# Performance work log

Measured on AMD Instinct MI355X. Metric: run time of the kernel, lower is better.

The kernel has to match this reference:

```python
import jax, jax.numpy as jnp
import numpy as np

B, N, D = 64, 256, 64          # datasets, samples per dataset, feature dim per variable (indim/2)
H, H2, OUT = 128, 64, 3        # hdlayers, hdlayers//2, outdim
REG, SIGMA, ALPHA = 1.0, 1.0, 2
BN_EPS = 1e-5


def _linear(k, fan_in, fan_out):
    kw, kb = jax.random.split(k)
    lim = 1.0 / np.sqrt(fan_in)
    w = jax.random.uniform(kw, (fan_in, fan_out), jnp.float32, -lim, lim)
    b = jax.random.uniform(kb, (fan_out,), jnp.float32, -lim, lim)
    return w, b


def setup_inputs() -> dict:
    key = jax.random.key(0)
    ks = jax.random.split(key, 10)
    w11_1, b11_1 = _linear(ks[2], D, H2)
    w11_2, b11_2 = _linear(ks[3], H2, H2)
    w12_1, b12_1 = _linear(ks[4], 2 * H2, H)
    w12_2, b12_2 = _linear(ks[5], H, H2)
    wc1, bc1 = _linear(ks[6], H2, OUT)
    w2, b2 = _linear(ks[7], OUT + 2, H2)
    wc2, bc2 = _linear(ks[8], H2, OUT)
    return {
        'x': jax.random.normal(ks[0], (B, N, D), jnp.float32),
        'y': jax.random.normal(ks[1], (B, N, D), jnp.float32),
        'w11_1': w11_1, 'b11_1': b11_1, 'w11_2': w11_2, 'b11_2': b11_2,
        'w12_1': w12_1, 'b12_1': b12_1, 'w12_2': w12_2, 'b12_2': b12_2,
        'wc1': wc1, 'bc1': bc1,
        'bn_gamma': jnp.ones((OUT + 2,), jnp.float32),
        'bn_beta': jnp.zeros((OUT + 2,), jnp.float32),
        'w2': w2, 'b2': b2, 'wc2': wc2, 'bc2': bc2,
    }


def _fro_normalize(t):
    # divide each [N, D] slice by its Frobenius norm
    return t / jnp.linalg.norm(t, axis=(1, 2), keepdims=True)


def _linear_regressor(x, y, reg):
    b, n, d = x.shape
    X = jnp.concatenate([jnp.ones((b, n, 1), x.dtype), x], axis=2)  # [B,N,d+1]
    P1 = jnp.einsum('bni,bnj->bij', X, X)                           # X^T X
    ridge = reg * jnp.eye(d + 1, dtype=x.dtype).at[0, 0].set(0.0)   # G^T G
    P2 = jnp.linalg.inv(P1 + ridge[None])
    P4 = X @ (P2 @ (jnp.swapaxes(X, 1, 2) @ y))
    loss = jnp.sum((y - P4) ** 2, axis=(1, 2))
    return loss, P4


def _gauss_kernel(x):
    # x: [B, N, F] -> [B, N, N]
    xn = jnp.sum(x * x, axis=-1)
    dist = xn[:, :, None] + xn[:, None, :] - 2.0 * jnp.einsum('bnd,bmd->bnm', x, x)
    return jnp.exp(-dist / SIGMA)


def _renyi_from_kernel(k):
    tr = jnp.trace(k, axis1=1, axis2=2)
    k = k / tr[:, None, None]
    ev = jnp.abs(jnp.linalg.eigvalsh(k))          # batched symeig eigenvalues
    return (1.0 / (1 - ALPHA)) * jnp.log2(jnp.sum(ev ** ALPHA, axis=-1))


def _renyi_mi(a, b):
    # batched normalized Renyi mutual information, a/b: [B, N, F]
    ka, kb = _gauss_kernel(a), _gauss_kernel(b)
    Hx = _renyi_from_kernel(ka)
    Hy = _renyi_from_kernel(kb)
    Hxy = _renyi_from_kernel(ka * kb)
    return (Hx + Hy - Hxy) / jnp.maximum(Hx, Hy)


def reference(x, y, w11_1, b11_1, w11_2, b11_2, w12_1, b12_1, w12_2, b12_2,
              wc1, bc1, bn_gamma, bn_beta, w2, b2, wc2, bc2):
    mlp11 = lambda t: jnp.maximum(t @ w11_1 + b11_1, 0.0) @ w11_2 + b11_2
    out_x = mlp11(x)                                  # [B,N,H2]
    out_y = mlp11(y)

    out_c = jnp.concatenate([out_x, out_y], axis=2)   # [B,N,2*H2]
    out_c = jnp.maximum(out_c @ w12_1 + b12_1, 0.0)
    out_c = jnp.maximum(out_c @ w12_2 + b12_2, 0.0)
    out_c = out_c.mean(axis=1)                        # [B,H2]
    out_c = out_c @ wc1 + bc1                         # [B,OUT]
    prob1 = jax.nn.softmax(out_c, axis=1)

    out_xn = _fro_normalize(out_x)
    out_yn = _fro_normalize(out_y)
    xx = _fro_normalize(x)
    yy = _fro_normalize(y)

    rx, px = _linear_regressor(out_xn, yy, REG)       # predict y from f(x)
    ry, py = _linear_regressor(out_yn, xx, REG)       # predict x from f(y)

    ex = _renyi_mi(yy - px, x)                        # [B]
    ey = _renyi_mi(xx - py, y)

    rxy = jnp.stack([ex, ey], axis=1)                 # [B,2]
    in_c = jnp.concatenate([out_c, rxy], axis=1)      # [B,OUT+2]
    mu = in_c.mean(axis=0)
    var = in_c.var(axis=0)                            # biased, as in torch BN training
    in_c = (in_c - mu) / jnp.sqrt(var + BN_EPS) * bn_gamma + bn_beta
    in_c = jnp.maximum(in_c @ w2 + b2, 0.0)
    out_c_f = in_c @ wc2 + bc2
    prob2 = jax.nn.softmax(out_c_f, axis=1)

    return (out_c, rx, ry, ex, ey, out_c_f, prob1, prob2)
```

## Files before the change

kernel.cpp:

```cpp
#include <hip/hip_runtime.h>
#include <math.h>

#define NB 64
#define NS 256
#define ND 64
#define NH2 64
#define NH 128
#define GSTRIDE 8448
#define WSTRIDE 4224


#define F4E(v_, e_) ((e_)==0?(v_).x:((e_)==1?(v_).y:((e_)==2?(v_).z:(v_).w)))

typedef __attribute__((ext_vector_type(8))) short bf16x8;
typedef __attribute__((ext_vector_type(4))) float f32x4;

__device__ __forceinline__ unsigned short f2bf(float f){
    union { float f; unsigned int u; } v; v.f = f;
    unsigned int r = v.u + 0x7fffu + ((v.u >> 16) & 1u);
    return (unsigned short)(r >> 16);
}
__device__ __forceinline__ float bf2f(unsigned short h){
    union { unsigned int u; float f; } v; v.u = ((unsigned int)h) << 16;
    return v.f;
}
__device__ __forceinline__ void sw2(unsigned short* ph, unsigned short* pl, int idx, float f){
    unsigned short h = f2bf(f);
    ph[idx] = h;
    pl[idx] = f2bf(f - bf2f(h));
}
__device__ __forceinline__ void sw2x2(unsigned short* ph, unsigned short* pl, int idx, float f0, float f1){
    unsigned short h0 = f2bf(f0), h1 = f2bf(f1);
    ushort2 hh; hh.x = h0; hh.y = h1;
    *(ushort2*)(ph + idx) = hh;
    ushort2 ll; ll.x = f2bf(f0 - bf2f(h0)); ll.y = f2bf(f1 - bf2f(h1));
    *(ushort2*)(pl + idx) = ll;
}

#define LD8(P_, row_, kb_) (*(const bf16x8*)((const char*)(P_) + (size_t)(row_)*144 + (kb_)))

__device__ __forceinline__ f32x4 mm64(
    const unsigned short* Ah, const unsigned short* Al,
    const unsigned short* Bh, const unsigned short* Bl,
    int ar, int br, int lrow, int lkb, f32x4 acc)
{
    const int ra = ar + lrow, rb = br + lrow;
    bf16x8 ah0 = LD8(Ah, ra, lkb), ah1 = LD8(Ah, ra, lkb+64);
    bf16x8 al0 = LD8(Al, ra, lkb), al1 = LD8(Al, ra, lkb+64);
    bf16x8 bh0 = LD8(Bh, rb, lkb), bh1 = LD8(Bh, rb, lkb+64);
    bf16x8 bl0 = LD8(Bl, rb, lkb), bl1 = LD8(Bl, rb, lkb+64);
    acc = __builtin_amdgcn_mfma_f32_16x16x32_bf16(ah0, bh0, acc, 0,0,0);
    acc = __builtin_amdgcn_mfma_f32_16x16x32_bf16(ah1, bh1, acc, 0,0,0);
    acc = __builtin_amdgcn_mfma_f32_16x16x32_bf16(ah0, bl0, acc, 0,0,0);
    acc = __builtin_amdgcn_mfma_f32_16x16x32_bf16(ah1, bl1, acc, 0,0,0);
    acc = __builtin_amdgcn_mfma_f32_16x16x32_bf16(al0, bh0, acc, 0,0,0);
    acc = __builtin_amdgcn_mfma_f32_16x16x32_bf16(al1, bh1, acc, 0,0,0);
    return acc;
}

__global__ __launch_bounds__(256) void k1_fused(
    const float* __restrict__ x, const float* __restrict__ y,
    const float* __restrict__ w11_1, const float* __restrict__ b11_1,
    const float* __restrict__ w11_2, const float* __restrict__ b11_2,
    const float* __restrict__ w12_1, const float* __restrict__ b12_1,
    const float* __restrict__ w12_2, const float* __restrict__ b12_2,
    float* __restrict__ out_x, float* __restrict__ out_y,
    float* __restrict__ mean_part)
{
    const int b = blockIdx.x >> 2, tile = blockIdx.x & 3;
    const int t = threadIdx.x;
    const int lane = t & 63, wv = t >> 6;
    const int lrow = lane & 15;
    const int lkb  = (lane >> 4) * 16;
    const int row0g = b*NS + tile*64;

    __shared__ unsigned short XYh[9216], XYl[9216];
    __shared__ unsigned short W1h[4608], W1l[4608];
    __shared__ unsigned short W2h[4608], W2l[4608];
    __shared__ unsigned short Hh [9216], Hl [9216];
    __shared__ unsigned short Oh [9216], Ol [9216];
    __shared__ float msum[4*68];

    #pragma unroll
    for (int u=0;u<8;u++){
        int id = t + 256*u;
        int r = id>>4, c0 = (id&15)*4;
        const float* src = (r < 64) ? (x + ((size_t)(row0g + r))*ND)
                                    : (y + ((size_t)(row0g + r - 64))*ND);
        float4 v = *(const float4*)(src + c0);
        sw2x2(XYh, XYl, r*72 + c0,   v.x, v.y);
        sw2x2(XYh, XYl, r*72 + c0+2, v.z, v.w);
    }
    #pragma unroll
    for (int u=0;u<2;u++){
        int id = t + 256*u;
        int rp = id>>4, c0 = (id&15)*4;
        float4 a0 = *(const float4*)(w11_1 + (size_t)(2*rp  )*64 + c0);
        float4 a1 = *(const float4*)(w11_1 + (size_t)(2*rp+1)*64 + c0);
        float4 b0 = *(const float4*)(w11_2 + (size_t)(2*rp  )*64 + c0);
        float4 b1 = *(const float4*)(w11_2 + (size_t)(2*rp+1)*64 + c0);
        #pragma unroll
        for (int i2=0;i2<4;i2++){
            sw2x2(W1h, W1l, (c0+i2)*72 + 2*rp, F4E(a0,i2), F4E(a1,i2));
            sw2x2(W2h, W2l, (c0+i2)*72 + 2*rp, F4E(b0,i2), F4E(b1,i2));
        }
    }
    __syncthreads();

    #pragma unroll
    for (int it=0; it<2; it++){
        const int ar = 32*wv + 16*it;
        #pragma unroll
        for (int jt=0; jt<4; jt++){
            float bb = b11_1[jt*16 + lrow];
            f32x4 acc = {bb,bb,bb,bb};
            acc = mm64(XYh, XYl, W1h, W1l, ar, jt*16, lrow, lkb, acc);
            #pragma unroll
            for (int e=0;e<4;e++){
                int row = ar + (lane>>4)*4 + e;
                int col = jt*16 + lrow;
                sw2(Hh, Hl, row*72 + col, fmaxf(acc[e], 0.f));
            }
        }
    }
    __syncthreads();

    #pragma unroll
    for (int u=0;u<4;u++){
        int id = t + 256*u;
        int krp = id>>5, c0 = (id&31)*4;
        float4 v0 = *(const float4*)(w12_1 + (size_t)(2*krp  )*NH + c0);
        float4 v1 = *(const float4*)(w12_1 + (size_t)(2*krp+1)*NH + c0);
        #pragma unroll
        for (int i2=0;i2<4;i2++)
            sw2x2(XYh, XYl, (c0+i2)*72 + 2*krp, F4E(v0,i2), F4E(v1,i2));
    }
    #pragma unroll
    for (int it=0; it<2; it++){
        const int ar = 32*wv + 16*it;
        #pragma unroll
        for (int jt=0; jt<4; jt++){
            float bb = b11_2[jt*16 + lrow];
            f32x4 acc = {bb,bb,bb,bb};
            acc = mm64(Hh, Hl, W2h, W2l, ar, jt*16, lrow, lkb, acc);
            #pragma unroll
            for (int e=0;e<4;e++){
                int row = ar + (lane>>4)*4 + e;
                int col = jt*16 + lrow;
                float v = acc[e];
                sw2(Oh, Ol, row*72 + col, v);
                float* dst = (row < 64) ? out_x : out_y;
                dst[((size_t)(row0g + (row & 63)))*NH2 + col] = v;
            }
        }
    }
    __syncthreads();

    f32x4 acc3[8];
    #pragma unroll
    for (int jt=0; jt<8; jt++){
        float bb = b12_1[jt*16 + lrow];
        f32x4 v = {bb,bb,bb,bb};
        acc3[jt] = v;
    }
    #pragma unroll
    for (int jt=0; jt<8; jt++)
        acc3[jt] = mm64(Oh, Ol, XYh, XYl, 16*wv, jt*16, lrow, lkb, acc3[jt]);
    __syncthreads();

    #pragma unroll
    for (int u=0;u<4;u++){
        int id = t + 256*u;
        int krp = id>>5, c0 = (id&31)*4;
        float4 v0 = *(const float4*)(w12_1 + (size_t)(64+2*krp  )*NH + c0);
        float4 v1 = *(const float4*)(w12_1 + (size_t)(64+2*krp+1)*NH + c0);
        #pragma unroll
        for (int i2=0;i2<4;i2++)
            sw2x2(XYh, XYl, (c0+i2)*72 + 2*krp, F4E(v0,i2), F4E(v1,i2));
    }
    #pragma unroll
    for (int u=0;u<2;u++){
        int id = t + 256*u;
        int krp = id>>4, c0 = (id&15)*4;
        float4 h0a = *(const float4*)(w12_2 + (size_t)(2*krp  )*NH2 + c0);
        float4 h0b = *(const float4*)(w12_2 + (size_t)(2*krp+1)*NH2 + c0);
        float4 h1a = *(const float4*)(w12_2 + (size_t)(64+2*krp  )*NH2 + c0);
        float4 h1b = *(const float4*)(w12_2 + (size_t)(64+2*krp+1)*NH2 + c0);
        #pragma unroll
        for (int i2=0;i2<4;i2++){
            sw2x2(W2h, W2l, (c0+i2)*72 + 2*krp, F4E(h0a,i2), F4E(h0b,i2));
            sw2x2(W1h, W1l, (c0+i2)*72 + 2*krp, F4E(h1a,i2), F4E(h1b,i2));
        }
    }
    __syncthreads();

    #pragma unroll
    for (int jt=0; jt<8; jt++)
        acc3[jt] = mm64(Oh, Ol, XYh, XYl, 64 + 16*wv, jt*16, lrow, lkb, acc3[jt]);
    #pragma unroll
    for (int jt=0; jt<8; jt++){
        #pragma unroll
        for (int e=0;e<4;e++){
            int row = 16*wv + (lane>>4)*4 + e;
            int col = jt*16 + lrow;
            float v = fmaxf(acc3[jt][e], 0.f);
            int idx = (col < 64) ? (row*72 + col) : ((64+row)*72 + (col-64));
            sw2(Hh, Hl, idx, v);
        }
    }
    __syncthreads();

    {
        f32x4 acc2[4];
        #pragma unroll
        for (int jt=0; jt<4; jt++){
            float bb = b12_2[jt*16 + lrow];
            f32x4 v = {bb,bb,bb,bb};
            acc2[jt] = v;
        }
        #pragma unroll
        for (int jt=0; jt<4; jt++){
            acc2[jt] = mm64(Hh, Hl, W2h, W2l, 16*wv,      jt*16, lrow, lkb, acc2[jt]);
            acc2[jt] = mm64(Hh, Hl, W1h, W1l, 64 + 16*wv, jt*16, lrow, lkb, acc2[jt]);
        }
        #pragma unroll
        for (int jt=0; jt<4; jt++){
            float s = fmaxf(acc2[jt][0],0.f) + fmaxf(acc2[jt][1],0.f)
                    + fmaxf(acc2[jt][2],0.f) + fmaxf(acc2[jt][3],0.f);
            s += __shfl_down(s, 32);
            s += __shfl_down(s, 16);
            if (lane < 16) msum[wv*68 + jt*16 + lane] = s;
        }
    }
    __syncthreads();
    if (t < 64){
        float ss = msum[t] + msum[68+t] + msum[2*68+t] + msum[3*68+t];
        mean_part[((size_t)(b*4+tile))*64 + t] = ss;
    }
}

__global__ __launch_bounds__(256) void k2a_build(
    const float* __restrict__ fx, const float* __restrict__ fy,
    const float* __restrict__ x, const float* __restrict__ y,
    float* __restrict__ gram)
{
    const int blk = blockIdx.x;
    const int kh = blk & 1, side = (blk>>1)&1, b = blk>>2;
    const float* feat = side ? fy : fx;
    const float* targ = side ? x : y;
    float* g = gram + (size_t)blk*GSTRIDE;
    const int t = threadIdx.x;
    const int ig2 = t & 15, jg2 = t >> 4;
    const int i0 = ig2*4, j0 = jg2*4;
    __shared__ float Zt[64*68], Tt[64*68];
    __shared__ float red[4];

    float accA[4][4], accR[4][4];
    #pragma unroll
    for (int u=0;u<4;u++)
        #pragma unroll
        for (int v=0;v<4;v++){ accA[u][v]=0.f; accR[u][v]=0.f; }
    float szp=0.f, stp=0.f, tsqp=0.f;
    const int cc_ = t & 63, rq = t >> 6;

    for (int sub=0; sub<2; sub++){
        if (sub) __syncthreads();
        const int r0g = b*NS + kh*128 + sub*64;
        #pragma unroll
        for (int u=0;u<4;u++){
            int id = t + 256*u; int r = id>>4, c4 = (id&15)*4;
            *(float4*)(Zt + r*68 + c4) = *(const float4*)(feat + ((size_t)(r0g+r))*NH2 + c4);
            *(float4*)(Tt + r*68 + c4) = *(const float4*)(targ + ((size_t)(r0g+r))*ND + c4);
        }
        __syncthreads();
        #pragma unroll
        for (int ch=0; ch<16; ch++){
            const int r0 = ch*4;
            float4 zi[4], zj[4], tj[4];
            #pragma unroll
            for (int c=0;c<4;c++){
                zi[c] = *(const float4*)(Zt + (r0+c)*68 + i0);
                zj[c] = *(const float4*)(Zt + (r0+c)*68 + j0);
                tj[c] = *(const float4*)(Tt + (r0+c)*68 + j0);
            }
            #pragma unroll
            for (int c=0;c<4;c++){
                #pragma unroll
                for (int u=0;u<4;u++){
                    const float zv = F4E(zi[c], u);
                    const float4 a4 = zj[c], r4 = tj[c];
                    accA[u][0] += zv*a4.x; accA[u][1] += zv*a4.y;
                    accA[u][2] += zv*a4.z; accA[u][3] += zv*a4.w;
                    accR[u][0] += zv*r4.x; accR[u][1] += zv*r4.y;
                    accR[u][2] += zv*r4.z; accR[u][3] += zv*r4.w;
                }
            }
        }
        #pragma unroll
        for (int rr=0; rr<16; rr++){
            int r = rq*16 + rr;
            szp += Zt[r*68 + cc_];
            float tv = Tt[r*68 + cc_];
            stp += tv; tsqp += tv*tv;
        }
    }
    #pragma unroll
    for (int u=0;u<4;u++){
        *(float4*)(g + (i0+u)*64 + j0) = make_float4(accA[u][0],accA[u][1],accA[u][2],accA[u][3]);
        *(float4*)(g + 4096 + (i0+u)*64 + j0) = make_float4(accR[u][0],accR[u][1],accR[u][2],accR[u][3]);
    }
    __syncthreads();
    Zt[rq*68 + cc_] = szp;
    Tt[rq*68 + cc_] = stp;
    float tq = tsqp;
    #pragma unroll
    for (int off=32; off; off>>=1) tq += __shfl_down(tq, off);
    if ((t&63)==0) red[t>>6] = tq;
    __syncthreads();
    if (t < 64){
        g[8192+t] = Zt[t] + Zt[68+t] + Zt[2*68+t] + Zt[3*68+t];
        g[8256+t] = Tt[t] + Tt[68+t] + Tt[2*68+t] + Tt[3*68+t];
    }
    if (t==0) g[8320] = red[0]+red[1]+red[2]+red[3];
}

__global__ __launch_bounds__(256) void k2b_solve(
    const float* __restrict__ gram, float* __restrict__ wbuf)
{
    const int bs = blockIdx.x;
    const float* g0 = gram + (size_t)(bs*2+0)*GSTRIDE;
    const float* g1 = gram + (size_t)(bs*2+1)*GSTRIDE;
    float* wb = wbuf + (size_t)bs*WSTRIDE;
    const int t = threadIdx.x;
    const int lane = t & 63, wv = t >> 6;
    const int lrow = lane & 15;
    const int lkb  = (lane >> 4) * 16;

    __shared__ float Rf[64*68];
    __shared__ float Wf[64*68];
    __shared__ unsigned short Eh[4608], El[4608];
    __shared__ unsigned short Wth[2][4608], Wtl[2][4608];
    __shared__ float szs[64], sts[64];
    __shared__ float sc[8];

    #pragma unroll
    for (int u=0;u<16;u++){
        int id = t + 256*u; int r = id>>6, c = id&63;
        Wf[r*68+c] = g0[id] + g1[id];
        Rf[r*68+c] = g0[4096+id] + g1[4096+id];
    }
    if (t<64){ szs[t] = g0[8192+t]+g1[8192+t]; sts[t] = g0[8256+t]+g1[8256+t]; }
    if (t==0) sc[1] = g0[8320]+g1[8320];
    __syncthreads();
    if (t<64){
        float dg = Wf[t*68+t];
        #pragma unroll
        for (int off=32; off; off>>=1) dg += __shfl_down(dg, off);
        if (t==0){ sc[0] = 1.0f/sqrtf(dg); sc[1] = 1.0f/sqrtf(sc[1]); }
    }
    __syncthreads();
    const float zinv = sc[0], tinv = sc[1];
    const float z2 = zinv*zinv, zt = zinv*tinv, inv256 = 1.0f/256.0f;
    const float i23 = 2.0f/3.0f;
    const int i = t>>2, qd = t&3;
    {
        const float szi = szs[i];
        #pragma unroll
        for (int q=0;q<4;q++){
            const int j = qd*16 + q*4;
            float4 a4 = *(const float4*)(Wf + i*68 + j);
            float4 sj = *(const float4*)(szs + j);
            float v0 = z2*(a4.x - szi*sj.x*inv256);
            float v1 = z2*(a4.y - szi*sj.y*inv256);
            float v2 = z2*(a4.z - szi*sj.z*inv256);
            float v3 = z2*(a4.w - szi*sj.w*inv256);
            if (i == j)   v0 += 1.f;
            else if (i == j+1) v1 += 1.f;
            else if (i == j+2) v2 += 1.f;
            else if (i == j+3) v3 += 1.f;
            float e0 = v0*i23 - ((i==j  ) ? 1.f : 0.f);
            float e1 = v1*i23 - ((i==j+1) ? 1.f : 0.f);
            float e2 = v2*i23 - ((i==j+2) ? 1.f : 0.f);
            float e3 = v3*i23 - ((i==j+3) ? 1.f : 0.f);
            sw2x2(Eh, El, i*72 + j,   e0, e1);
            sw2x2(Eh, El, i*72 + j+2, e2, e3);
            float4 rv = *(float4*)(Rf + i*68 + j);
            float4 t4 = *(const float4*)(sts + j);
            float r0 = zt*(rv.x - szi*t4.x*inv256)*i23;
            float r1 = zt*(rv.y - szi*t4.y*inv256)*i23;
            float r2 = zt*(rv.z - szi*t4.z*inv256)*i23;
            float r3 = zt*(rv.w - szi*t4.w*inv256)*i23;
            *(float4*)(Rf + i*68 + j) = make_float4(r0,r1,r2,r3);
            sw2(Wth[0], Wtl[0], (j  )*72 + i, r0);
            sw2(Wth[0], Wtl[0], (j+1)*72 + i, r1);
            sw2(Wth[0], Wtl[0], (j+2)*72 + i, r2);
            sw2(Wth[0], Wtl[0], (j+3)*72 + i, r3);
        }
    }
    __syncthreads();

    int cur = 0;
    for (int n=0; n<12; n++){
        f32x4 acc[4];
        #pragma unroll
        for (int jt=0; jt<4; jt++){
            f32x4 zz = {0.f,0.f,0.f,0.f};
            acc[jt] = mm64(Eh, El, Wth[cur], Wtl[cur], 16*wv, jt*16, lrow, lkb, zz);
        }
        const int gi0 = 16*wv + (lane>>4)*4;
        #pragma unroll
        for (int jt=0; jt<4; jt++){
            const int gj = jt*16 + lrow;
            float w0 = Rf[(gi0  )*68 + gj] - acc[jt][0];
            float w1 = Rf[(gi0+1)*68 + gj] - acc[jt][1];
            float w2 = Rf[(gi0+2)*68 + gj] - acc[jt][2];
            float w3 = Rf[(gi0+3)*68 + gj] - acc[jt][3];
            sw2x2(Wth[cur^1], Wtl[cur^1], gj*72 + gi0,   w0, w1);
            sw2x2(Wth[cur^1], Wtl[cur^1], gj*72 + gi0+2, w2, w3);
            if (n == 11){
                Wf[(gi0  )*68 + gj] = w0;  wb[(gi0  )*64 + gj] = w0;
                Wf[(gi0+1)*68 + gj] = w1;  wb[(gi0+1)*64 + gj] = w1;
                Wf[(gi0+2)*68 + gj] = w2;  wb[(gi0+2)*64 + gj] = w2;
                Wf[(gi0+3)*68 + gj] = w3;  wb[(gi0+3)*64 + gj] = w3;
            }
        }
        cur ^= 1;
        __syncthreads();
    }

    if (t < 64){
        float s = 0.f;
        for (int i2=0; i2<64; i2++) s += szs[i2]*Wf[i2*68 + t];
        wb[4096+t] = (tinv*sts[t] - zinv*s) * inv256;
    }
    if (t==0){ wb[4160] = zinv; wb[4161] = tinv; }
}

__global__ __launch_bounds__(256) void k2c_resid(
    const float* __restrict__ fx, const float* __restrict__ fy,
    const float* __restrict__ x, const float* __restrict__ y,
    const float* __restrict__ wbuf,
    float* __restrict__ resx, float* __restrict__ resy,
    float* __restrict__ resn, float* __restrict__ rawn,
    float* __restrict__ loss_part,
    unsigned short* __restrict__ resbf, unsigned short* __restrict__ tgbf)
{
    const int blk = blockIdx.x;
    const int h = blk & 1, side = (blk>>1)&1, b = blk>>2;
    const float* feat = side ? fy : fx;
    const float* targ = side ? x : y;
    float* res = side ? resy : resx;
    const float* wb = wbuf + (size_t)(b*2+side)*WSTRIDE;
    const int t = threadIdx.x;
    const int ig = t>>4, jg = t&15, d0 = jg*4;
    const int row0 = b*NS + h*128;
    __shared__ float sZ[128*68];
    __shared__ float sW[64*68];
    __shared__ float c0s[64];
    __shared__ float rnp[128*17];
    __shared__ float rqp[128*17];
    __shared__ float red[4];

    #pragma unroll
    for (int u=0;u<8;u++){
        int id = t + 256*u; int r = id>>4, c4 = (id&15)*4;
        *(float4*)(sZ + r*68 + c4) = *(const float4*)(feat + ((size_t)(row0+r))*NH2 + c4);
    }
    #pragma unroll
    for (int u=0;u<4;u++){
        int id = t + 256*u; int r = id>>4, c4 = (id&15)*4;
        *(float4*)(sW + r*68 + c4) = *(const float4*)(wb + (size_t)r*64 + c4);
    }
    if (t<64) c0s[t] = wb[4096+t];
    const float zinv = wb[4160], tinv = wb[4161];
    __syncthreads();

    float acc[8][4];
    #pragma unroll
    for (int u=0;u<8;u++){ acc[u][0]=0.f; acc[u][1]=0.f; acc[u][2]=0.f; acc[u][3]=0.f; }
    #pragma unroll
    for (int ch=0; ch<16; ch++){
        const int k0 = ch*4;
        float4 wr[4];
        #pragma unroll
        for (int c=0;c<4;c++) wr[c] = *(const float4*)(sW + (k0+c)*68 + d0);
        #pragma unroll
        for (int u=0;u<8;u++){
            float4 zv = *(const float4*)(sZ + (ig+16*u)*68 + k0);
            #pragma unroll
            for (int c=0;c<4;c++){
                const float zc = F4E(zv, c);
                const float4 w4 = wr[c];
                acc[u][0] += zc*w4.x; acc[u][1] += zc*w4.y;
                acc[u][2] += zc*w4.z; acc[u][3] += zc*w4.w;
            }
        }
    }
    const float4 c04 = *(const float4*)(c0s + d0);
    #pragma unroll
    for (int u=0;u<8;u++){
        const int r = ig + 16*u;
        const int gr = row0 + r;
        float4 q = *(const float4*)(targ + (size_t)gr*ND + d0);
        float4 rr;
        rr.x = tinv*q.x - zinv*acc[u][0] - c04.x;
        rr.y = tinv*q.y - zinv*acc[u][1] - c04.y;
        rr.z = tinv*q.z - zinv*acc[u][2] - c04.z;
        rr.w = tinv*q.w - zinv*acc[u][3] - c04.w;
        *(float4*)(res + (size_t)gr*ND + d0) = rr;
        *(ushort4*)(resbf + ((size_t)side*NB*NS + gr)*64 + d0) =
            make_ushort4(f2bf(rr.x), f2bf(rr.y), f2bf(rr.z), f2bf(rr.w));
        *(ushort4*)(tgbf + ((size_t)side*NB*NS + gr)*64 + d0) =
            make_ushort4(f2bf(q.x), f2bf(q.y), f2bf(q.z), f2bf(q.w));
        rnp[r*17 + jg] = rr.x*rr.x + rr.y*rr.y + rr.z*rr.z + rr.w*rr.w;
        rqp[r*17 + jg] = q.x*q.x + q.y*q.y + q.z*q.z + q.w*q.w;
    }
    __syncthreads();
    float myrn = 0.f;
    if (t < 128){
        float rn=0.f, rq=0.f;
        #pragma unroll
        for (int g2=0; g2<16; g2++){ rn += rnp[t*17+g2]; rq += rqp[t*17+g2]; }
        resn[(size_t)(side*NB+b)*NS + h*128 + t] = rn;
        rawn[(size_t)(side*NB+b)*NS + h*128 + t] = rq;
        myrn = rn;
    }
    float l = myrn;
    #pragma unroll
    for (int off=32; off; off>>=1) l += __shfl_down(l, off);
    if ((t&63)==0) red[t>>6] = l;
    __syncthreads();
    if (t==0) loss_part[blk] = red[0]+red[1]+red[2]+red[3];
}

__global__ __launch_bounds__(256) void k3_renyi(
    const unsigned short* __restrict__ resbf, const unsigned short* __restrict__ tgbf,
    const float* __restrict__ resn, const float* __restrict__ rawn,
    float* __restrict__ part3)
{
    const int blk = blockIdx.x;
    const int jh = blk & 1;
    const int b = (blk >> 1) & (NB-1);
    const int side = (blk >> 1) >> 6;
    const unsigned short* Am = resbf + ((size_t)side*NB*NS + (size_t)b*NS)*64;
    const unsigned short* Bm = tgbf  + ((size_t)(1-side)*NB*NS + (size_t)b*NS)*64;
    const float* nA = resn + (size_t)(side*NB+b)*NS;
    const float* nB = rawn + (size_t)((1-side)*NB+b)*NS;
    const int t = threadIdx.x;
    const int lane = t & 63, wv = t >> 6;

    __shared__ unsigned short Abf[256*72];
    __shared__ unsigned short Bbf[256*72];
    __shared__ float nAs[256], nBs[256];
    __shared__ float red[4][3];

    #pragma unroll
    for (int u=0;u<8;u++){
        int id = t + 256*u;
        int r = id>>3, c = id&7;
        *(float4*)((char*)Abf + r*144 + c*16) = *(const float4*)(Am + (size_t)r*64 + c*8);
        *(float4*)((char*)Bbf + r*144 + c*16) = *(const float4*)(Bm + (size_t)r*64 + c*8);
    }
    nAs[t] = nA[t];
    nBs[t] = nB[t];
    __syncthreads();

    const int lrow = lane & 15;
    const int lkb  = (lane >> 4) * 16;
    const char* pA = (const char*)Abf;
    const char* pB = (const char*)Bbf;
    const f32x4 zero4 = {0.f, 0.f, 0.f, 0.f};
    const float CEXP = -2.8853900817779268f;

    float Sa=0.f, Sb=0.f, Sab=0.f;
    #pragma unroll
    for (int it=0; it<4; it++){
        const int i0 = wv*64 + it*16;
        const int arow = i0 + lrow;
        bf16x8 aA0 = *(const bf16x8*)(pA + arow*144 + lkb);
        bf16x8 aA1 = *(const bf16x8*)(pA + arow*144 + lkb + 64);
        bf16x8 aB0 = *(const bf16x8*)(pB + arow*144 + lkb);
        bf16x8 aB1 = *(const bf16x8*)(pB + arow*144 + lkb + 64);
        float nAi[4], nBi[4];
        #pragma unroll
        for (int e=0;e<4;e++){
            int gi = i0 + (lane>>4)*4 + e;
            nAi[e] = nAs[gi]; nBi[e] = nBs[gi];
        }
        #pragma unroll
        for (int jt=0; jt<8; jt++){
            const int j0 = jh*128 + jt*16;
            const int brow = j0 + lrow;
            bf16x8 bA0 = *(const bf16x8*)(pA + brow*144 + lkb);
            bf16x8 bA1 = *(const bf16x8*)(pA + brow*144 + lkb + 64);
            bf16x8 bB0 = *(const bf16x8*)(pB + brow*144 + lkb);
            bf16x8 bB1 = *(const bf16x8*)(pB + brow*144 + lkb + 64);
            f32x4 cA = __builtin_amdgcn_mfma_f32_16x16x32_bf16(aA0, bA0, zero4, 0, 0, 0);
            cA = __builtin_amdgcn_mfma_f32_16x16x32_bf16(aA1, bA1, cA, 0, 0, 0);
            f32x4 cB = __builtin_amdgcn_mfma_f32_16x16x32_bf16(aB0, bB0, zero4, 0, 0, 0);
            cB = __builtin_amdgcn_mfma_f32_16x16x32_bf16(aB1, bB1, cB, 0, 0, 0);
            const int gj = j0 + lrow;
            const float nAj = nAs[gj], nBj = nBs[gj];
            #pragma unroll
            for (int e=0;e<4;e++){
                const int gi = i0 + (lane>>4)*4 + e;
                const float dda = (gi==gj) ? 0.f : (nAi[e] + nAj - 2.f*cA[e]);
                const float ddb = (gi==gj) ? 0.f : (nBi[e] + nBj - 2.f*cB[e]);
                const float ka2 = exp2f(CEXP*dda);
                const float kb2 = exp2f(CEXP*ddb);
                Sa += ka2; Sb += kb2; Sab += ka2*kb2;
            }
        }
    }
    #pragma unroll
    for (int off=32; off; off>>=1){
        Sa += __shfl_down(Sa,off); Sb += __shfl_down(Sb,off); Sab += __shfl_down(Sab,off);
    }
    if (lane==0){ red[wv][0]=Sa; red[wv][1]=Sb; red[wv][2]=Sab; }
    __syncthreads();
    if (t==0){
        float* o = part3 + (size_t)blk*3;
        o[0] = red[0][0]+red[1][0]+red[2][0]+red[3][0];
        o[1] = red[0][1]+red[1][1]+red[2][1]+red[3][1];
        o[2] = red[0][2]+red[1][2]+red[2][2]+red[3][2];
    }
}

__global__ __launch_bounds__(64) void k4_final(
    const float* __restrict__ mean_part, const float* __restrict__ part3,
    const float* __restrict__ loss_part,
    const float* __restrict__ wc1, const float* __restrict__ bc1,
    const float* __restrict__ bn_gamma, const float* __restrict__ bn_beta,
    const float* __restrict__ w2, const float* __restrict__ b2,
    const float* __restrict__ wc2, const float* __restrict__ bc2,
    float* __restrict__ dout)
{
    const int t = threadIdx.x;
    __shared__ float ic[64][5];
    __shared__ float mu[5], iv[5];

    dout[192+t] = loss_part[4*t+0] + loss_part[4*t+1];
    dout[256+t] = loss_part[4*t+2] + loss_part[4*t+3];

    float o0 = bc1[0], o1 = bc1[1], o2 = bc1[2];
    for (int c=0;c<64;c++){
        float mv = mean_part[(t*4+0)*64+c] + mean_part[(t*4+1)*64+c]
                 + mean_part[(t*4+2)*64+c] + mean_part[(t*4+3)*64+c];
        mv *= (1.0f/256.0f);
        o0 += mv*wc1[c*3+0]; o1 += mv*wc1[c*3+1]; o2 += mv*wc1[c*3+2];
    }
    dout[t*3+0]=o0; dout[t*3+1]=o1; dout[t*3+2]=o2;
    {
        float m = fmaxf(o0,fmaxf(o1,o2));
        float e0=__expf(o0-m), e1=__expf(o1-m), e2=__expf(o2-m);
        float inv = 1.f/(e0+e1+e2);
        dout[640+t*3+0]=e0*inv; dout[640+t*3+1]=e1*inv; dout[640+t*3+2]=e2*inv;
    }
    float exy[2];
    #pragma unroll
    for (int side=0; side<2; side++){
        const float* pp = part3 + (size_t)((side*NB + t)*2)*3;
        float Sa = pp[0]+pp[3];
        float Sb = pp[1]+pp[4];
        float Sab= pp[2]+pp[5];
        float Hx  = 16.f - log2f(Sa);
        float Hy  = 16.f - log2f(Sb);
        float Hxy = 16.f - log2f(Sab);
        float mi = (Hx + Hy - Hxy) / fmaxf(Hx, Hy);
        dout[(side?384:320)+t] = mi;
        exy[side] = mi;
    }
    ic[t][0]=o0; ic[t][1]=o1; ic[t][2]=o2; ic[t][3]=exy[0]; ic[t][4]=exy[1];
    __syncthreads();
    if (t<5){
        float m=0.f;
        for (int bb=0;bb<64;bb++) m += ic[bb][t];
        m *= (1.f/64.f);
        float v=0.f;
        for (int bb=0;bb<64;bb++){ float d=ic[bb][t]-m; v+=d*d; }
        v *= (1.f/64.f);
        mu[t]=m; iv[t]=1.f/sqrtf(v+1e-5f);
    }
    __syncthreads();
    float vn[5];
    #pragma unroll
    for (int c=0;c<5;c++) vn[c] = (ic[t][c]-mu[c])*iv[c]*bn_gamma[c]+bn_beta[c];
    float q0=bc2[0], q1=bc2[1], q2=bc2[2];
    for (int j=0;j<64;j++){
        float hh = b2[j];
        #pragma unroll
        for (int c=0;c<5;c++) hh += vn[c]*w2[c*64+j];
        hh = fmaxf(hh,0.f);
        q0 += hh*wc2[j*3+0]; q1 += hh*wc2[j*3+1]; q2 += hh*wc2[j*3+2];
    }
    dout[448+t*3+0]=q0; dout[448+t*3+1]=q1; dout[448+t*3+2]=q2;
    float m = fmaxf(q0,fmaxf(q1,q2));
    float e0=__expf(q0-m), e1=__expf(q1-m), e2=__expf(q2-m);
    float inv=1.f/(e0+e1+e2);
    dout[832+t*3+0]=e0*inv; dout[832+t*3+1]=e1*inv; dout[832+t*3+2]=e2*inv;
}

extern "C" void kernel_launch(void* const* d_in, const int* in_sizes, int n_in,
                              void* d_out, int out_size, void* d_ws, size_t ws_size,
                              hipStream_t stream)
{
    const float* x     = (const float*)d_in[0];
    const float* y     = (const float*)d_in[1];
    const float* w11_1 = (const float*)d_in[2];
    const float* b11_1 = (const float*)d_in[3];
    const float* w11_2 = (const float*)d_in[4];
    const float* b11_2 = (const float*)d_in[5];
    const float* w12_1 = (const float*)d_in[6];
    const float* b12_1 = (const float*)d_in[7];
    const float* w12_2 = (const float*)d_in[8];
    const float* b12_2 = (const float*)d_in[9];
    const float* wc1   = (const float*)d_in[10];
    const float* bc1   = (const float*)d_in[11];
    const float* bn_g  = (const float*)d_in[12];
    const float* bn_b  = (const float*)d_in[13];
    const float* w2    = (const float*)d_in[14];
    const float* b2    = (const float*)d_in[15];
    const float* wc2   = (const float*)d_in[16];
    const float* bc2   = (const float*)d_in[17];

    float* ws   = (float*)d_ws;
    float* dout = (float*)d_out;
    float* out_x = ws;
    float* out_y = ws + 1048576;
    float* resx  = ws + 2097152;
    float* resy  = ws + 3145728;
    float* resn  = ws + 4194304;
    float* rawn  = resn + 32768;
    float* mean_part = rawn + 32768;
    float* part3 = mean_part + 16384;
    float* loss_part = part3 + 3840;
    float* gram  = ws + 4280320;
    float* wbuf  = gram + 2162688;
    unsigned short* resbf = (unsigned short*)gram;
    unsigned short* tgbf  = resbf + 2097152;

    hipLaunchKernelGGL(k1_fused, dim3(NB*4), dim3(256), 0, stream,
        x,y,w11_1,b11_1,w11_2,b11_2,w12_1,b12_1,w12_2,b12_2,
        out_x,out_y,mean_part);
    hipLaunchKernelGGL(k2a_build, dim3(NB*4), dim3(256), 0, stream,
        out_x,out_y,x,y,gram);
    hipLaunchKernelGGL(k2b_solve, dim3(2*NB), dim3(256), 0, stream,
        gram,wbuf);
    hipLaunchKernelGGL(k2c_resid, dim3(NB*4), dim3(256), 0, stream,
        out_x,out_y,x,y,wbuf,resx,resy,resn,rawn,loss_part,resbf,tgbf);
    hipLaunchKernelGGL(k3_renyi, dim3(NB*2*2), dim3(256), 0, stream,
        resbf,tgbf,resn,rawn,part3);
    hipLaunchKernelGGL(k4_final, dim3(1), dim3(64), 0, stream,
        mean_part,part3,loss_part,wc1,bc1,bn_g,bn_b,w2,b2,wc2,bc2,dout);
}
```

Before: 88.48 us.

## Fuse residual computation into Renyi kernel with split-bf16 MFMA regression

Merges the residual kernel and the Renyi kernel into one, kRG. Each block recomputes the full 256-row residual of its dataset in shared memory using MFMA with hi/lo bf16-split operands, instead of reading bf16 residuals written to global memory by a separate launch. It also computes row norms and the regression loss in place, removing the global round-trip for resbf/tgbf/resn/rawn and one launch. In exchange, each of the two jh blocks per dataset redundantly computes the whole residual, and norms are now taken from bf16-rounded values.

```diff
diff --git a/kernel.cpp b/kernel.cpp
--- a/kernel.cpp
+++ b/kernel.cpp
@@ -436,139 +436,130 @@
     if (t==0){ wb[4160] = zinv; wb[4161] = tinv; }
 }
 
-__global__ __launch_bounds__(256) void k2c_resid(
+__global__ __launch_bounds__(256) void kRG(
     const float* __restrict__ fx, const float* __restrict__ fy,
     const float* __restrict__ x, const float* __restrict__ y,
     const float* __restrict__ wbuf,
-    float* __restrict__ resx, float* __restrict__ resy,
-    float* __restrict__ resn, float* __restrict__ rawn,
-    float* __restrict__ loss_part,
-    unsigned short* __restrict__ resbf, unsigned short* __restrict__ tgbf)
-{
-    const int blk = blockIdx.x;
-    const int h = blk & 1, side = (blk>>1)&1, b = blk>>2;
-    const float* feat = side ? fy : fx;
-    const float* targ = side ? x : y;
-    float* res = side ? resy : resx;
-    const float* wb = wbuf + (size_t)(b*2+side)*WSTRIDE;
-    const int t = threadIdx.x;
-    const int ig = t>>4, jg = t&15, d0 = jg*4;
-    const int row0 = b*NS + h*128;
-    __shared__ float sZ[128*68];
-    __shared__ float sW[64*68];
-    __shared__ float c0s[64];
-    __shared__ float rnp[128*17];
-    __shared__ float rqp[128*17];
-    __shared__ float red[4];
-
-    #pragma unroll
-    for (int u=0;u<8;u++){
-        int id = t + 256*u; int r = id>>4, c4 = (id&15)*4;
-        *(float4*)(sZ + r*68 + c4) = *(const float4*)(feat + ((size_t)(row0+r))*NH2 + c4);
-    }
-    #pragma unroll
-    for (int u=0;u<4;u++){
-        int id = t + 256*u; int r = id>>4, c4 = (id&15)*4;
-        *(float4*)(sW + r*68 + c4) = *(const float4*)(wb + (size_t)r*64 + c4);
-    }
-    if (t<64) c0s[t] = wb[4096+t];
-    const float zinv = wb[4160], tinv = wb[4161];
-    __syncthreads();
-
-    float acc[8][4];
-    #pragma unroll
-    for (int u=0;u<8;u++){ acc[u][0]=0.f; acc[u][1]=0.f; acc[u][2]=0.f; acc[u][3]=0.f; }
-    #pragma unroll
-    for (int ch=0; ch<16; ch++){
-        const int k0 = ch*4;
-        float4 wr[4];
-        #pragma unroll
-        for (int c=0;c<4;c++) wr[c] = *(const float4*)(sW + (k0+c)*68 + d0);
-        #pragma unroll
-        for (int u=0;u<8;u++){
-            float4 zv = *(const float4*)(sZ + (ig+16*u)*68 + k0);
-            #pragma unroll
-            for (int c=0;c<4;c++){
-                const float zc = F4E(zv, c);
-                const float4 w4 = wr[c];
-                acc[u][0] += zc*w4.x; acc[u][1] += zc*w4.y;
-                acc[u][2] += zc*w4.z; acc[u][3] += zc*w4.w;
-            }
-        }
-    }
-    const float4 c04 = *(const float4*)(c0s + d0);
-    #pragma unroll
-    for (int u=0;u<8;u++){
-        const int r = ig + 16*u;
-        const int gr = row0 + r;
-        float4 q = *(const float4*)(targ + (size_t)gr*ND + d0);
-        float4 rr;
-        rr.x = tinv*q.x - zinv*acc[u][0] - c04.x;
-        rr.y = tinv*q.y - zinv*acc[u][1] - c04.y;
-        rr.z = tinv*q.z - zinv*acc[u][2] - c04.z;
-        rr.w = tinv*q.w - zinv*acc[u][3] - c04.w;
-        *(float4*)(res + (size_t)gr*ND + d0) = rr;
-        *(ushort4*)(resbf + ((size_t)side*NB*NS + gr)*64 + d0) =
-            make_ushort4(f2bf(rr.x), f2bf(rr.y), f2bf(rr.z), f2bf(rr.w));
-        *(ushort4*)(tgbf + ((size_t)side*NB*NS + gr)*64 + d0) =
-            make_ushort4(f2bf(q.x), f2bf(q.y), f2bf(q.z), f2bf(q.w));
-        rnp[r*17 + jg] = rr.x*rr.x + rr.y*rr.y + rr.z*rr.z + rr.w*rr.w;
-        rqp[r*17 + jg] = q.x*q.x + q.y*q.y + q.z*q.z + q.w*q.w;
-    }
-    __syncthreads();
-    float myrn = 0.f;
-    if (t < 128){
-        float rn=0.f, rq=0.f;
-        #pragma unroll
-        for (int g2=0; g2<16; g2++){ rn += rnp[t*17+g2]; rq += rqp[t*17+g2]; }
-        resn[(size_t)(side*NB+b)*NS + h*128 + t] = rn;
-        rawn[(size_t)(side*NB+b)*NS + h*128 + t] = rq;
-        myrn = rn;
-    }
-    float l = myrn;
-    #pragma unroll
-    for (int off=32; off; off>>=1) l += __shfl_down(l, off);
-    if ((t&63)==0) red[t>>6] = l;
-    __syncthreads();
-    if (t==0) loss_part[blk] = red[0]+red[1]+red[2]+red[3];
-}
-
-__global__ __launch_bounds__(256) void k3_renyi(
-    const unsigned short* __restrict__ resbf, const unsigned short* __restrict__ tgbf,
-    const float* __restrict__ resn, const float* __restrict__ rawn,
-    float* __restrict__ part3)
+    float* __restrict__ part3, float* __restrict__ dout)
 {
     const int blk = blockIdx.x;
     const int jh = blk & 1;
     const int b = (blk >> 1) & (NB-1);
     const int side = (blk >> 1) >> 6;
-    const unsigned short* Am = resbf + ((size_t)side*NB*NS + (size_t)b*NS)*64;
-    const unsigned short* Bm = tgbf  + ((size_t)(1-side)*NB*NS + (size_t)b*NS)*64;
-    const float* nA = resn + (size_t)(side*NB+b)*NS;
-    const float* nB = rawn + (size_t)((1-side)*NB+b)*NS;
+    const float* feat = side ? fy : fx;
+    const float* targ = side ? x : y;
+    const float* bmat = side ? y : x;
+    const float* wb = wbuf + (size_t)(b*2+side)*WSTRIDE;
     const int t = threadIdx.x;
     const int lane = t & 63, wv = t >> 6;
-
-    __shared__ unsigned short Abf[256*72];
-    __shared__ unsigned short Bbf[256*72];
+    const int lrow = lane & 15, lkb = (lane>>4)*16;
+
+    __shared__ unsigned short resA[256*72];
+    __shared__ unsigned short tgB [256*72];
+    __shared__ unsigned short Zh[2*4608], Zl[2*4608];
+    __shared__ unsigned short Wth[4608], Wtl[4608];
+    __shared__ float c0s[64];
     __shared__ float nAs[256], nBs[256];
     __shared__ float red[4][3];
-
-    #pragma unroll
-    for (int u=0;u<8;u++){
+    __shared__ float lred[4];
+
+    #pragma unroll
+    for (int u=0;u<4;u++){
         int id = t + 256*u;
-        int r = id>>3, c = id&7;
-        *(float4*)((char*)Abf + r*144 + c*16) = *(const float4*)(Am + (size_t)r*64 + c*8);
-        *(float4*)((char*)Bbf + r*144 + c*16) = *(const float4*)(Bm + (size_t)r*64 + c*8);
-    }
-    nAs[t] = nA[t];
-    nBs[t] = nB[t];
-    __syncthreads();
-
-    const int lrow = lane & 15;
-    const int lkb  = (lane >> 4) * 16;
-    const char* pA = (const char*)Abf;
-    const char* pB = (const char*)Bbf;
+        int k = id>>4, c0 = (id&15)*4;
+        float4 v = *(const float4*)(wb + (size_t)k*64 + c0);
+        sw2(Wth, Wtl, (c0+0)*72 + k, v.x);
+        sw2(Wth, Wtl, (c0+1)*72 + k, v.y);
+        sw2(Wth, Wtl, (c0+2)*72 + k, v.z);
+        sw2(Wth, Wtl, (c0+3)*72 + k, v.w);
+    }
+    if (t<64) c0s[t] = wb[4096+t];
+    const float zinv = wb[4160], tinv = wb[4161];
+    #pragma unroll
+    for (int u=0;u<16;u++){
+        int id = t + 256*u;
+        int r = id>>4, c0 = (id&15)*4;
+        float4 v = *(const float4*)(bmat + ((size_t)(b*NS+r))*ND + c0);
+        ushort4 h;
+        h.x=f2bf(v.x); h.y=f2bf(v.y); h.z=f2bf(v.z); h.w=f2bf(v.w);
+        *(ushort4*)(tgB + r*72 + c0) = h;
+    }
+    #pragma unroll
+    for (int u=0;u<4;u++){
+        int id = t + 256*u;
+        int r = id>>4, c0 = (id&15)*4;
+        float4 v = *(const float4*)(feat + ((size_t)(b*NS + r))*NH2 + c0);
+        sw2x2(Zh, Zl, r*72+c0,   v.x, v.y);
+        sw2x2(Zh, Zl, r*72+c0+2, v.z, v.w);
+    }
+    __syncthreads();
+
+    float lacc = 0.f;
+    for (int c=0; c<4; c++){
+        if (c < 3){
+            unsigned short* zh = Zh + ((c+1)&1)*4608;
+            unsigned short* zl = Zl + ((c+1)&1)*4608;
+            #pragma unroll
+            for (int u=0;u<4;u++){
+                int id = t + 256*u;
+                int r = id>>4, c0 = (id&15)*4;
+                float4 v = *(const float4*)(feat + ((size_t)(b*NS + (c+1)*64 + r))*NH2 + c0);
+                sw2x2(zh, zl, r*72+c0,   v.x, v.y);
+                sw2x2(zh, zl, r*72+c0+2, v.z, v.w);
+            }
+        }
+        const unsigned short* zh = Zh + (c&1)*4608;
+        const unsigned short* zl = Zl + (c&1)*4608;
+        f32x4 acc[4];
+        #pragma unroll
+        for (int jt=0; jt<4; jt++){
+            f32x4 zz = {0.f,0.f,0.f,0.f};
+            acc[jt] = mm64(zh, zl, Wth, Wtl, 16*wv, jt*16, lrow, lkb, zz);
+        }
+        const int r0 = 16*wv + (lane>>4)*4;
+        #pragma unroll
+        for (int jt=0; jt<4; jt++){
+            const int gj = jt*16 + lrow;
+            const float cc = c0s[gj];
+            #pragma unroll
+            for (int e=0;e<4;e++){
+                const int grow = c*64 + r0 + e;
+                float q = targ[((size_t)(b*NS+grow))*ND + gj];
+                float rr = tinv*q - zinv*acc[jt][e] - cc;
+                lacc += rr*rr;
+                resA[grow*72 + gj] = f2bf(rr);
+            }
+        }
+        __syncthreads();
+    }
+
+    {
+        float l = lacc;
+        #pragma unroll
+        for (int off=32; off; off>>=1) l += __shfl_down(l, off);
+        if (lane==0) lred[wv] = l;
+    }
+    {
+        float sa=0.f, sb=0.f;
+        #pragma unroll
+        for (int j8=0;j8<8;j8++){
+            bf16x8 va = *(const bf16x8*)((const char*)resA + (size_t)t*144 + j8*16);
+            bf16x8 vb = *(const bf16x8*)((const char*)tgB  + (size_t)t*144 + j8*16);
+            #pragma unroll
+            for (int e2=0;e2<8;e2++){
+                float fa = bf2f((unsigned short)va[e2]);
+                float fb = bf2f((unsigned short)vb[e2]);
+                sa += fa*fa; sb += fb*fb;
+            }
+        }
+        nAs[t] = sa; nBs[t] = sb;
+    }
+    __syncthreads();
+    if (t==0 && jh==0)
+        dout[(side?256:192)+b] = lred[0]+lred[1]+lred[2]+lred[3];
+
+    const char* pA = (const char*)resA;
+    const char* pB = (const char*)tgB;
     const f32x4 zero4 = {0.f, 0.f, 0.f, 0.f};
     const float CEXP = -2.8853900817779268f;
 
@@ -628,7 +619,6 @@
 
 __global__ __launch_bounds__(64) void k4_final(
     const float* __restrict__ mean_part, const float* __restrict__ part3,
-    const float* __restrict__ loss_part,
     const float* __restrict__ wc1, const float* __restrict__ bc1,
     const float* __restrict__ bn_gamma, const float* __restrict__ bn_beta,
     const float* __restrict__ w2, const float* __restrict__ b2,
@@ -638,9 +628,6 @@
     const int t = threadIdx.x;
     __shared__ float ic[64][5];
     __shared__ float mu[5], iv[5];
-
-    dout[192+t] = loss_part[4*t+0] + loss_part[4*t+1];
-    dout[256+t] = loss_part[4*t+2] + loss_part[4*t+3];
 
     float o0 = bc1[0], o1 = bc1[1], o2 = bc1[2];
     for (int c=0;c<64;c++){
@@ -727,17 +714,10 @@
     float* dout = (float*)d_out;
     float* out_x = ws;
     float* out_y = ws + 1048576;
-    float* resx  = ws + 2097152;
-    float* resy  = ws + 3145728;
-    float* resn  = ws + 4194304;
-    float* rawn  = resn + 32768;
-    float* mean_part = rawn + 32768;
+    float* mean_part = ws + 4259840;
     float* part3 = mean_part + 16384;
-    float* loss_part = part3 + 3840;
     float* gram  = ws + 4280320;
     float* wbuf  = gram + 2162688;
-    unsigned short* resbf = (unsigned short*)gram;
-    unsigned short* tgbf  = resbf + 2097152;
 
     hipLaunchKernelGGL(k1_fused, dim3(NB*4), dim3(256), 0, stream,
         x,y,w11_1,b11_1,w11_2,b11_2,w12_1,b12_1,w12_2,b12_2,
@@ -746,10 +726,8 @@
         out_x,out_y,x,y,gram);
     hipLaunchKernelGGL(k2b_solve, dim3(2*NB), dim3(256), 0, stream,
         gram,wbuf);
-    hipLaunchKernelGGL(k2c_resid, dim3(NB*4), dim3(256), 0, stream,
-        out_x,out_y,x,y,wbuf,resx,resy,resn,rawn,loss_part,resbf,tgbf);
-    hipLaunchKernelGGL(k3_renyi, dim3(NB*2*2), dim3(256), 0, stream,
-        resbf,tgbf,resn,rawn,part3);
+    hipLaunchKernelGGL(kRG, dim3(NB*2*2), dim3(256), 0, stream,
+        out_x,out_y,x,y,wbuf,part3,dout);
     hipLaunchKernelGGL(k4_final, dim3(1), dim3(64), 0, stream,
-        mean_part,part3,loss_part,wc1,bc1,bn_g,bn_b,w2,b2,wc2,bc2,dout);
-}
+        mean_part,part3,wc1,bc1,bn_g,bn_b,w2,b2,wc2,bc2,dout);
+}
```

Measured after the change: 85.25 us. -3.6%, faster.
